# Kernel optimization log

Measured on AMD Instinct MI355X. Metric: run time of the kernel, lower is better.

## Reference

```python
import jax, jax.numpy as jnp
import numpy as np

# Hard-coded dims from the module
D, L, R, H, M, T = 64, 90, 5760, 1024, 1024, 20
N_OUT = 3
B = 64  # per-timestep batch; feature has B*T rows


def setup_inputs() -> dict:
    key = jax.random.key(0)
    ks = jax.random.split(key, 20)
    def w(i, shape, fan_in):
        return jax.random.normal(ks[i], shape, dtype=jnp.float32) * (1.0 / np.sqrt(fan_in))
    return {
        "feature": jax.random.normal(ks[0], (B * T, L, D), dtype=jnp.float32),
        # additive attention params (alpha over L locations)
        "attn_Wx": w(1, (D, D), D),
        "attn_Wh": w(2, (H, D), H),
        "attn_v": w(3, (D,), D),
        # LSTM (PyTorch gate order i,f,g,o)
        "W_ih": w(4, (4 * H, R), R),
        "W_hh": w(5, (4 * H, H), H),
        "b_ih": jnp.zeros((4 * H,), jnp.float32),
        "b_hh": jnp.zeros((4 * H,), jnp.float32),
        # output head
        "Wh_w": w(6, (M, H), H),
        "Wh_b": jnp.zeros((M,), jnp.float32),
        "Wy_w": w(7, (M, R), R),
        "Wu_w": w(8, (N_OUT, M), M),
        "Wu_b": jnp.zeros((N_OUT,), jnp.float32),
        # LSTM-state initializers
        "iWh_w": w(9, (H, D), D),
        "iWh_b": jnp.zeros((H,), jnp.float32),
        "iWc_w": w(10, (H, D), D),
        "iWc_b": jnp.zeros((H,), jnp.float32),
    }


def reference(feature, attn_Wx, attn_Wh, attn_v, W_ih, W_hh, b_ih, b_hh,
              Wh_w, Wh_b, Wy_w, Wu_w, Wu_b, iWh_w, iWh_b, iWc_w, iWc_b):
    batch = feature.shape[0] // T
    seq = feature.reshape(batch, T, L, D).transpose(1, 0, 2, 3)  # [T,B,L,D]

    # initializeLSTM (no_grad in the original -> stop_gradient)
    f0 = jnp.mean(seq[0], axis=1)                                  # [B,D]
    h0 = jax.lax.stop_gradient(jnp.tanh(f0 @ iWh_w.T + iWh_b))     # [B,H]
    c0 = jax.lax.stop_gradient(jnp.tanh(f0 @ iWc_w.T + iWc_b))     # [B,H]

    def step(carry, xt):  # xt: [B,L,D]
        h, c = carry
        # additive attention over L locations
        e = jnp.tanh(jnp.einsum('bld,da->bla', xt, attn_Wx)
                     + (h @ attn_Wh)[:, None, :]) @ attn_v          # [B,L]
        alpha = jax.nn.softmax(e, axis=1)
        visual = (xt * alpha[:, :, None]).reshape(-1, R)            # [B,R]
        # single LSTM step (PyTorch gate order i,f,g,o)
        gates = visual @ W_ih.T + b_ih + h @ W_hh.T + b_hh          # [B,4H]
        i, f, g, o = jnp.split(gates, 4, axis=-1)
        c = jax.nn.sigmoid(f) * c + jax.nn.sigmoid(i) * jnp.tanh(g)
        h = jax.nn.sigmoid(o) * jnp.tanh(c)
        # ut = Wu(Wh(h) + Wy(visual)); dropout omitted for determinism
        ut = (h @ Wh_w.T + Wh_b + visual @ Wy_w.T) @ Wu_w.T + Wu_b  # [B,n_out]
        return (h, c), ut

    _, outs = jax.lax.scan(step, (h0, c0), seq)                     # [T,B,n_out]
    return outs.transpose(1, 0, 2).reshape(batch * T, -1)
```

## Files before the change

### kernel.cpp

```cpp
#include <hip/hip_runtime.h>
#include <math.h>

typedef _Float16 half8 __attribute__((ext_vector_type(8)));
typedef _Float16 half4v __attribute__((ext_vector_type(4)));
typedef _Float16 half2v __attribute__((ext_vector_type(2)));
typedef float floatx16 __attribute__((ext_vector_type(16)));

#define TT 20
#define NB 64
#define LL 90
#define DD 64
#define RR 5760
#define HH 1024
#define NG 4096
#define KT 6784
#define CH0 90
#define CHT 106
#define SPLITK 8

__device__ __forceinline__ float sigm(float x) { return 1.f / (1.f + expf(-x)); }

__global__ __launch_bounds__(256) void k_prep(const float* __restrict__ s1, _Float16* __restrict__ d1, int n1,
                                              const float* __restrict__ s2, _Float16* __restrict__ d2, int n2,
                                              int ncb, const float* __restrict__ Wh, _Float16* __restrict__ WhT) {
    const int bid = blockIdx.x, tid = threadIdx.x;
    if (bid >= ncb) {
        const int idx = (bid - ncb) * 256 + tid;
        const int a = idx >> 8, k4 = (idx & 255) * 4;
        half4v o;
#pragma unroll
        for (int u = 0; u < 4; ++u) o[u] = (_Float16)Wh[(size_t)(k4 + u) * DD + a];
        *(half4v*)(WhT + (size_t)a * HH + k4) = o;
        return;
    }
    int i = (bid * 256 + tid) * 4;
    const float* s; _Float16* d;
    if (i < n1) { s = s1 + i; d = d1 + i; }
    else if ((i -= n1) < n2) { s = s2 + i; d = d2 + i; }
    else return;
    const float4 v = *(const float4*)s;
    half4v o;
    o[0] = (_Float16)v.x; o[1] = (_Float16)v.y;
    o[2] = (_Float16)v.z; o[3] = (_Float16)v.w;
    *(half4v*)d = o;
}

__global__ __launch_bounds__(256) void k_xproj(const float* __restrict__ feat,
                                               const float* __restrict__ Wx,
                                               _Float16* __restrict__ xp) {
    __shared__ float sWx[DD * DD];
    __shared__ float sx[16 * DD];
    const int row = blockIdx.x;
    const int tid = threadIdx.x;
    for (int e = tid * 4; e < DD * DD; e += 1024)
        *(float4*)(sWx + e) = *(const float4*)(Wx + e);
    const int a4 = tid & 15, lg = tid >> 4;
    const float* frow = feat + (size_t)row * RR;
    for (int lb = 0; lb < LL; lb += 16) {
        __syncthreads();
        { int e = tid * 4; int ls = e >> 6, dd = e & 63;
          if (lb + ls < LL) *(float4*)(sx + e) = *(const float4*)(frow + (lb + ls) * DD + dd); }
        __syncthreads();
        const int l = lb + lg;
        if (l < LL) {
            float a0 = 0, a1 = 0, a2 = 0, a3 = 0;
            for (int dd = 0; dd < DD; ++dd) {
                const float xv = sx[lg * DD + dd];
                const float4 wv = *(const float4*)(sWx + dd * DD + a4 * 4);
                a0 += xv * wv.x; a1 += xv * wv.y; a2 += xv * wv.z; a3 += xv * wv.w;
            }
            half4v o;
            o[0] = (_Float16)a0; o[1] = (_Float16)a1; o[2] = (_Float16)a2; o[3] = (_Float16)a3;
            *(half4v*)(xp + (size_t)row * RR + l * DD + a4 * 4) = o;
        }
    }
}

__global__ __launch_bounds__(256) void k_init(const float* __restrict__ feat,
        const float* __restrict__ iWh_w, const float* __restrict__ iWh_b,
        const float* __restrict__ iWc_w, const float* __restrict__ iWc_b,
        float* __restrict__ h, float* __restrict__ c, _Float16* __restrict__ h16) {
    __shared__ float f0p[4][DD];
    __shared__ float f0[DD];
    const int b = blockIdx.x, tid = threadIdx.x;
    const int dd = tid & 63, lg = tid >> 6;
    const float* frow = feat + (size_t)(b * TT) * RR;
    float p = 0;
    for (int l = lg; l < LL; l += 4) p += frow[l * DD + dd];
    f0p[lg][dd] = p;
    __syncthreads();
    if (tid < DD) f0[tid] = (f0p[0][tid] + f0p[1][tid] + f0p[2][tid] + f0p[3][tid]) * (1.0f / LL);
    __syncthreads();
    for (int o = tid; o < HH; o += 256) {
        float ah = iWh_b[o], ac = iWc_b[o];
        for (int d0 = 0; d0 < DD; d0 += 4) {
            const float4 wh = *(const float4*)(iWh_w + (size_t)o * DD + d0);
            const float4 wc = *(const float4*)(iWc_w + (size_t)o * DD + d0);
            ah += f0[d0] * wh.x + f0[d0 + 1] * wh.y + f0[d0 + 2] * wh.z + f0[d0 + 3] * wh.w;
            ac += f0[d0] * wc.x + f0[d0 + 1] * wc.y + f0[d0 + 2] * wc.z + f0[d0 + 3] * wc.w;
        }
        const float hv = tanhf(ah), cv = tanhf(ac);
        h[b * HH + o] = hv; c[b * HH + o] = cv;
        h16[b * HH + o] = (_Float16)hv;
    }
}

__global__ __launch_bounds__(512) void k_step(int t, int do_cell,
        const float* __restrict__ gpart, const float* __restrict__ b_ih,
        const float* __restrict__ b_hh, const float* __restrict__ cin,
        float* __restrict__ cout, _Float16* __restrict__ h16,
        const float* __restrict__ h0buf, const float* __restrict__ feat,
        const _Float16* __restrict__ xp, const _Float16* __restrict__ WhT,
        const float* __restrict__ v, _Float16* __restrict__ V16,
        const _Float16* __restrict__ Wyu, float* __restrict__ vpart,
        float* __restrict__ hpart) {
    __shared__ float sh[HH];
    __shared__ float hWhp[8][DD];
    __shared__ float hWh[DD];
    __shared__ float sv[DD];
    __shared__ float ep[LL][4];
    __shared__ float se[128];
    __shared__ float red[128];
    __shared__ float salpha[LL];
    __shared__ float hdr[8][6];
    const int b = blockIdx.x, tid = threadIdx.x;
    if (tid < DD) sv[tid] = v[tid];
    float hp0 = 0.f, hp1 = 0.f, hp2 = 0.f;
    float vp0 = 0.f, vp1 = 0.f, vp2 = 0.f;

    if (do_cell) {
        const int j0 = tid * 2;
        float ag[4][2];
#pragma unroll
        for (int g = 0; g < 4; ++g) { ag[g][0] = 0.f; ag[g][1] = 0.f; }
#pragma unroll
        for (int sp = 0; sp < SPLITK; ++sp) {
            const float* P = gpart + ((size_t)sp * NB + b) * NG;
#pragma unroll
            for (int g = 0; g < 4; ++g) {
                const float2 pv = *(const float2*)(P + g * HH + j0);
                ag[g][0] += pv.x; ag[g][1] += pv.y;
            }
        }
#pragma unroll
        for (int g = 0; g < 4; ++g) {
            const float2 bi = *(const float2*)(b_ih + g * HH + j0);
            const float2 bh = *(const float2*)(b_hh + g * HH + j0);
            ag[g][0] += bi.x + bh.x; ag[g][1] += bi.y + bh.y;
        }
        const float2 cold = *(const float2*)(cin + (size_t)b * HH + j0);
        float co[2] = { cold.x, cold.y };
        float2 cnew; half2v hh2;
#pragma unroll
        for (int q = 0; q < 2; ++q) {
            const float cv = sigm(ag[1][q]) * co[q] + sigm(ag[0][q]) * tanhf(ag[2][q]);
            const float hv = sigm(ag[3][q]) * tanhf(cv);
            ((float*)&cnew)[q] = cv;
            hh2[q] = (_Float16)hv;
            sh[j0 + q] = hv;
        }
        *(float2*)(cout + (size_t)b * HH + j0) = cnew;
        *(half2v*)(h16 + (size_t)b * HH + j0) = hh2;
        const float h0f = (float)hh2[0], h1f = (float)hh2[1];
        hp0 = h0f * (float)Wyu[0 * KT + RR + j0] + h1f * (float)Wyu[0 * KT + RR + j0 + 1];
        hp1 = h0f * (float)Wyu[1 * KT + RR + j0] + h1f * (float)Wyu[1 * KT + RR + j0 + 1];
        hp2 = h0f * (float)Wyu[2 * KT + RR + j0] + h1f * (float)Wyu[2 * KT + RR + j0 + 1];
    } else {
        for (int e = tid; e < HH; e += 512) sh[e] = h0buf[(size_t)b * HH + e];
    }
    __syncthreads();

    if (t < TT) {
        { const int a = tid & 63, q8 = tid >> 6;
          const _Float16* Wq = WhT + (size_t)a * HH + q8 * 128;
          const float* shq = sh + q8 * 128;
          float p = 0.f;
#pragma unroll
          for (int k = 0; k < 128; k += 8) {
              const half8 wv = *(const half8*)(Wq + k);
#pragma unroll
              for (int u = 0; u < 8; ++u) p += shq[k + u] * (float)wv[u];
          }
          hWhp[q8][a] = p; }
        __syncthreads();
        if (tid < DD) {
            float s = 0.f;
#pragma unroll
            for (int q = 0; q < 8; ++q) s += hWhp[q][tid];
            hWh[tid] = s;
        }
        __syncthreads();

        const size_t frow = (size_t)(b * TT + t) * RR;
        if (tid < 360) {
            const int l = tid >> 2, qq = tid & 3;
            const _Float16* xr = xp + frow + l * DD + qq * 16;
            const half8 x0 = *(const half8*)(xr);
            const half8 x1 = *(const half8*)(xr + 8);
            float acc = 0.f;
#pragma unroll
            for (int i = 0; i < 8; ++i)
                acc += tanhf((float)x0[i] + hWh[qq * 16 + i]) * sv[qq * 16 + i];
#pragma unroll
            for (int i = 0; i < 8; ++i)
                acc += tanhf((float)x1[i] + hWh[qq * 16 + 8 + i]) * sv[qq * 16 + 8 + i];
            ep[l][qq] = acc;
        }
        __syncthreads();
        if (tid < LL) se[tid] = ep[tid][0] + ep[tid][1] + ep[tid][2] + ep[tid][3];
        else if (tid < 128) se[tid] = -1e30f;
        __syncthreads();
        if (tid < 128) red[tid] = se[tid];
        __syncthreads();
        for (int s = 64; s; s >>= 1) { if (tid < s) red[tid] = fmaxf(red[tid], red[tid + s]); __syncthreads(); }
        const float mx = red[0];
        __syncthreads();
        float ex = 0.f;
        if (tid < LL) { ex = expf(se[tid] - mx); salpha[tid] = ex; }
        if (tid < 128) red[tid] = ex;
        __syncthreads();
        for (int s = 64; s; s >>= 1) { if (tid < s) red[tid] += red[tid + s]; __syncthreads(); }
        const float inv = 1.f / red[0];
        __syncthreads();
        if (tid < LL) salpha[tid] *= inv;
        __syncthreads();

        _Float16* vout = V16 + (size_t)b * RR;
        const float* fr = feat + frow;
        for (int e = tid * 4; e < RR; e += 2048) {
            const float4 u4 = *(const float4*)(fr + e);
            const float al = salpha[e >> 6];
            half4v o;
            o[0] = (_Float16)(u4.x * al); o[1] = (_Float16)(u4.y * al);
            o[2] = (_Float16)(u4.z * al); o[3] = (_Float16)(u4.w * al);
            *(half4v*)(vout + e) = o;
            const half4v w0 = *(const half4v*)(Wyu + e);
            const half4v w1 = *(const half4v*)(Wyu + KT + e);
            const half4v w2 = *(const half4v*)(Wyu + 2 * KT + e);
#pragma unroll
            for (int u = 0; u < 4; ++u) {
                const float xv = (float)o[u];
                vp0 += xv * (float)w0[u]; vp1 += xv * (float)w1[u]; vp2 += xv * (float)w2[u];
            }
        }
    }

    for (int o = 32; o; o >>= 1) {
        hp0 += __shfl_down(hp0, o, 64); hp1 += __shfl_down(hp1, o, 64); hp2 += __shfl_down(hp2, o, 64);
        vp0 += __shfl_down(vp0, o, 64); vp1 += __shfl_down(vp1, o, 64); vp2 += __shfl_down(vp2, o, 64);
    }
    if ((tid & 63) == 0) {
        const int w = tid >> 6;
        hdr[w][0] = hp0; hdr[w][1] = hp1; hdr[w][2] = hp2;
        hdr[w][3] = vp0; hdr[w][4] = vp1; hdr[w][5] = vp2;
    }
    __syncthreads();
    if (tid < 6) {
        float s = 0.f;
#pragma unroll
        for (int w = 0; w < 8; ++w) s += hdr[w][tid];
        if (tid < 3) { if (do_cell) hpart[((size_t)(t - 1) * NB + b) * 3 + tid] = s; }
        else         { if (t < TT)  vpart[((size_t)t * NB + b) * 3 + (tid - 3)] = s; }
    }
}

__device__ __forceinline__ void stage_tile(const char* src, size_t stride, char* lds, int ln) {
    const char* g = src + (size_t)(ln >> 3) * stride + (((ln & 7) ^ (ln >> 3)) << 4);
#pragma unroll
    for (int i = 0; i < 8; ++i)
        __builtin_amdgcn_global_load_lds(
            (const __attribute__((address_space(1))) void*)(g + (size_t)(i * 8) * stride),
            (__attribute__((address_space(3))) void*)(lds + i * 1024), 16, 0, 0);
}

struct Src2 { const char* p0; size_t s0; const char* p1; size_t s1; };

__device__ __forceinline__ const char* chunk_ptr(const Src2& s, int c, size_t& stride) {
    if (c < CH0) { stride = s.s0; return s.p0 + (size_t)c * 128; }
    stride = s.s1; return s.p1 + (size_t)(c - CH0) * 128;
}

__global__ __launch_bounds__(128) void k_gates(const _Float16* __restrict__ V16,
        const _Float16* __restrict__ h16, const _Float16* __restrict__ Wih,
        const _Float16* __restrict__ Whh, float* __restrict__ gpart) {
    __shared__ char smem[65536];
    const int bid = blockIdx.x;
    const int kb = bid >> 6;
    const int nt = ((bid & 7) << 3) | ((bid >> 3) & 7);
    const int tid = threadIdx.x, w = tid >> 6, ln = tid & 63;
    char* wlds = smem + w * 32768;

    Src2 As = { (const char*)V16, (size_t)RR * 2, (const char*)h16, (size_t)HH * 2 };
    Src2 Bs = { (const char*)(Wih + (size_t)(nt * 64) * RR), (size_t)RR * 2,
                (const char*)(Whh + (size_t)(nt * 64) * HH), (size_t)HH * 2 };

    floatx16 acc00, acc01, acc10, acc11;
#pragma unroll
    for (int i = 0; i < 16; ++i) { acc00[i] = 0.f; acc01[i] = 0.f; acc10[i] = 0.f; acc11[i] = 0.f; }

    const int start = kb * 2 + w;
    const int r = ln & 31;
    const int xsw = (r & 7) << 4;
    const int fo = (ln >> 5) * 16;
    const int rbyte = r * 128;

    int c = start, bsel = 0;
    { size_t st; const char* p = chunk_ptr(As, c, st); stage_tile(p, st, wlds, ln);
      p = chunk_ptr(Bs, c, st); stage_tile(p, st, wlds + 8192, ln); }
    while (true) {
        const int cn = c + 16;
        if (cn < CHT) {
            char* nl = wlds + ((bsel ^ 1) << 14);
            size_t st; const char* p = chunk_ptr(As, cn, st); stage_tile(p, st, nl, ln);
            p = chunk_ptr(Bs, cn, st); stage_tile(p, st, nl + 8192, ln);
            asm volatile("s_waitcnt vmcnt(16)" ::: "memory");
        } else {
            asm volatile("s_waitcnt vmcnt(0)" ::: "memory");
        }
        __builtin_amdgcn_sched_barrier(0);
        const char* LA = wlds + (bsel << 14);
        const char* LB = LA + 8192;
#pragma unroll
        for (int kk = 0; kk < 4; ++kk) {
            const int o = ((kk * 32 + fo) ^ xsw);
            const half8 a0 = *(const half8*)(LA + rbyte + o);
            const half8 a1 = *(const half8*)(LA + 4096 + rbyte + o);
            const half8 b0 = *(const half8*)(LB + rbyte + o);
            const half8 b1 = *(const half8*)(LB + 4096 + rbyte + o);
            acc00 = __builtin_amdgcn_mfma_f32_32x32x16_f16(a0, b0, acc00, 0, 0, 0);
            acc01 = __builtin_amdgcn_mfma_f32_32x32x16_f16(a0, b1, acc01, 0, 0, 0);
            acc10 = __builtin_amdgcn_mfma_f32_32x32x16_f16(a1, b0, acc10, 0, 0, 0);
            acc11 = __builtin_amdgcn_mfma_f32_32x32x16_f16(a1, b1, acc11, 0, 0, 0);
        }
        if (cn >= CHT) break;
        c = cn; bsel ^= 1;
    }
    __syncthreads();
    float* Rg = (float*)(smem + w * 16384);
    const int rbase = 4 * (ln >> 5), lr = ln & 31;
#pragma unroll
    for (int q = 0; q < 16; ++q) {
        const int row = rbase + (q & 3) + 8 * (q >> 2);
        Rg[row * 64 + lr]             = acc00[q];
        Rg[row * 64 + 32 + lr]        = acc01[q];
        Rg[(row + 32) * 64 + lr]      = acc10[q];
        Rg[(row + 32) * 64 + 32 + lr] = acc11[q];
    }
    __syncthreads();
    const float* R0 = (const float*)smem;
    const float* R1 = (const float*)(smem + 16384);
    float* Cout = gpart + (size_t)kb * (NB * NG);
    for (int e = tid * 4; e < 4096; e += 512) {
        const float4 u = *(const float4*)(R0 + e);
        const float4 v2 = *(const float4*)(R1 + e);
        float4 s2; s2.x = u.x + v2.x; s2.y = u.y + v2.y; s2.z = u.z + v2.z; s2.w = u.w + v2.w;
        const int row = e >> 6, col = e & 63;
        *(float4*)(Cout + (size_t)row * NG + nt * 64 + col) = s2;
    }
}

__global__ __launch_bounds__(256) void k_wfuse(const float* __restrict__ Wy,
        const float* __restrict__ Whw, const float* __restrict__ Wu,
        const float* __restrict__ Whb, const float* __restrict__ Wub,
        _Float16* __restrict__ Wyu16, float* __restrict__ cst) {
    __shared__ float sWu[3 * HH];
    __shared__ float part[4][3][64];
    const int tid = threadIdx.x;
    for (int e = tid * 4; e < 3 * HH; e += 1024)
        *(float4*)(sWu + e) = *(const float4*)(Wu + e);
    __syncthreads();
    if (blockIdx.x == CHT) {
        float a0 = 0, a1 = 0, a2 = 0;
        for (int m = tid; m < HH; m += 256) {
            const float wb = Whb[m];
            a0 += sWu[m] * wb; a1 += sWu[HH + m] * wb; a2 += sWu[2 * HH + m] * wb;
        }
        __shared__ float rp[3][256];
        rp[0][tid] = a0; rp[1][tid] = a1; rp[2][tid] = a2;
        __syncthreads();
        for (int s = 128; s; s >>= 1) {
            if (tid < s) { rp[0][tid] += rp[0][tid + s]; rp[1][tid] += rp[1][tid + s]; rp[2][tid] += rp[2][tid + s]; }
            __syncthreads();
        }
        if (tid < 3) cst[tid] = rp[tid][0] + Wub[tid];
        return;
    }
    const int kk = tid & 63, qm = tid >> 6;
    const int k = blockIdx.x * 64 + kk;
    const float* src; size_t ld;
    if (blockIdx.x < CH0) { src = Wy + k; ld = RR; }
    else { src = Whw + (k - RR); ld = HH; }
    float a0 = 0, a1 = 0, a2 = 0;
    for (int m = qm * 256; m < qm * 256 + 256; ++m) {
        const float val = src[(size_t)m * ld];
        a0 += sWu[m] * val; a1 += sWu[HH + m] * val; a2 += sWu[2 * HH + m] * val;
    }
    part[qm][0][kk] = a0; part[qm][1][kk] = a1; part[qm][2][kk] = a2;
    __syncthreads();
    if (tid < 192) {
        const int j = tid >> 6, k2 = tid & 63;
        const float s = part[0][j][k2] + part[1][j][k2] + part[2][j][k2] + part[3][j][k2];
        Wyu16[(size_t)j * KT + blockIdx.x * 64 + k2] = (_Float16)s;
    }
}

__global__ __launch_bounds__(256) void k_fin(const float* __restrict__ vpart,
        const float* __restrict__ hpart, const float* __restrict__ cst,
        float* __restrict__ out) {
    const int idx = blockIdx.x * 256 + threadIdx.x;
    if (idx >= TT * NB * 3) return;
    const int r = idx / 3, j = idx - r * 3;
    const int ts = r >> 6, b = r & 63;
    out[((size_t)b * TT + ts) * 3 + j] = vpart[idx] + hpart[idx] + cst[j];
}

extern "C" void kernel_launch(void* const* d_in, const int* in_sizes, int n_in,
                              void* d_out, int out_size, void* d_ws, size_t ws_size,
                              hipStream_t stream) {
    (void)in_sizes; (void)n_in; (void)out_size;
    const float* feature = (const float*)d_in[0];
    const float* attn_Wx = (const float*)d_in[1];
    const float* attn_Wh = (const float*)d_in[2];
    const float* attn_v  = (const float*)d_in[3];
    const float* W_ih    = (const float*)d_in[4];
    const float* W_hh    = (const float*)d_in[5];
    const float* b_ih    = (const float*)d_in[6];
    const float* b_hh    = (const float*)d_in[7];
    const float* Wh_w    = (const float*)d_in[8];
    const float* Wh_b    = (const float*)d_in[9];
    const float* Wy_w    = (const float*)d_in[10];
    const float* Wu_w    = (const float*)d_in[11];
    const float* Wu_b    = (const float*)d_in[12];
    const float* iWh_w   = (const float*)d_in[13];
    const float* iWh_b   = (const float*)d_in[14];
    const float* iWc_w   = (const float*)d_in[15];
    const float* iWc_b   = (const float*)d_in[16];
    float* out = (float*)d_out;

    char* ws = (char*)d_ws;
    size_t off = 0;
    auto alloc = [&](size_t bytes) { void* p = ws + off; off += (bytes + 255) & ~(size_t)255; return p; };
    _Float16* Wih16 = (_Float16*)alloc((size_t)NG * RR * 2);
    _Float16* Whh16 = (_Float16*)alloc((size_t)NG * HH * 2);
    _Float16* WhT16 = (_Float16*)alloc((size_t)DD * HH * 2);
    _Float16* xp16  = (_Float16*)alloc((size_t)1280 * RR * 2);
    _Float16* V16   = (_Float16*)alloc((size_t)NB * RR * 2);
    float*    hbuf  = (float*)alloc((size_t)NB * HH * 4);
    float*    cb0   = (float*)alloc((size_t)NB * HH * 4);
    float*    cb1   = (float*)alloc((size_t)NB * HH * 4);
    _Float16* h16   = (_Float16*)alloc((size_t)NB * HH * 2);
    float*    gpart = (float*)alloc((size_t)SPLITK * NB * NG * 4);
    _Float16* Wyu16 = (_Float16*)alloc((size_t)3 * KT * 2);
    float*    vpart = (float*)alloc((size_t)TT * NB * 3 * 4);
    float*    hpart = (float*)alloc((size_t)TT * NB * 3 * 4);
    float*    cstb  = (float*)alloc(16);
    if (ws_size < off) return;

    const int nconv = NG * RR + NG * HH;
    const int ncb = (nconv / 4 + 255) / 256;
    k_prep<<<ncb + 64, 256, 0, stream>>>(W_ih, Wih16, NG * RR, W_hh, Whh16, NG * HH,
                                         ncb, attn_Wh, WhT16);
    k_xproj<<<1280, 256, 0, stream>>>(feature, attn_Wx, xp16);
    k_wfuse<<<CHT + 1, 256, 0, stream>>>(Wy_w, Wh_w, Wu_w, Wh_b, Wu_b, Wyu16, cstb);
    k_init<<<64, 256, 0, stream>>>(feature, iWh_w, iWh_b, iWc_w, iWc_b, hbuf, cb0, h16);

    k_step<<<64, 512, 0, stream>>>(0, 0, gpart, b_ih, b_hh, cb0, cb1, h16, hbuf,
                                   feature, xp16, WhT16, attn_v, V16, Wyu16,
                                   vpart, hpart);
    for (int t = 0; t < TT; ++t) {
        k_gates<<<512, 128, 0, stream>>>(V16, h16, Wih16, Whh16, gpart);
        const float* cin = (t & 1) ? cb1 : cb0;
        float* cou       = (t & 1) ? cb0 : cb1;
        k_step<<<64, 512, 0, stream>>>(t + 1, 1, gpart, b_ih, b_hh, cin, cou, h16, hbuf,
                                       feature, xp16, WhT16, attn_v, V16, Wyu16,
                                       vpart, hpart);
    }

    k_fin<<<15, 256, 0, stream>>>(vpart, hpart, cstb, out);
}
```

Measured before the change: 687.3 us.

## Overlap per-step Wx projection with gate GEMM and merge prep kernels

The full 1280-row Wx projection is no longer precomputed up front. Each gates launch now gets 64 extra blocks that compute the next timestep's projection into a double-buffered 64-row slice, overlapping it with the GEMM. The gate GEMM is restructured into 128 blocks of 4 waves that share a staged A tile and write split-K partials directly, and the small prep kernels and the final output kernel are folded into one prep launch and into the last step. This cuts launch count and prep work, but puts extra projection work on the per-step critical path and lowers GEMM block parallelism from 512 to 128 blocks.

```diff
diff --git a/kernel.cpp b/kernel.cpp
--- a/kernel.cpp
+++ b/kernel.cpp
@@ -20,20 +20,9 @@
 
 __device__ __forceinline__ float sigm(float x) { return 1.f / (1.f + expf(-x)); }
 
-__global__ __launch_bounds__(256) void k_prep(const float* __restrict__ s1, _Float16* __restrict__ d1, int n1,
-                                              const float* __restrict__ s2, _Float16* __restrict__ d2, int n2,
-                                              int ncb, const float* __restrict__ Wh, _Float16* __restrict__ WhT) {
-    const int bid = blockIdx.x, tid = threadIdx.x;
-    if (bid >= ncb) {
-        const int idx = (bid - ncb) * 256 + tid;
-        const int a = idx >> 8, k4 = (idx & 255) * 4;
-        half4v o;
-#pragma unroll
-        for (int u = 0; u < 4; ++u) o[u] = (_Float16)Wh[(size_t)(k4 + u) * DD + a];
-        *(half4v*)(WhT + (size_t)a * HH + k4) = o;
-        return;
-    }
-    int i = (bid * 256 + tid) * 4;
+__global__ __launch_bounds__(256) void k_conv2(const float* __restrict__ s1, _Float16* __restrict__ d1, int n1,
+                                               const float* __restrict__ s2, _Float16* __restrict__ d2, int n2) {
+    int i = (blockIdx.x * 256 + threadIdx.x) * 4;
     const float* s; _Float16* d;
     if (i < n1) { s = s1 + i; d = d1 + i; }
     else if ((i -= n1) < n2) { s = s2 + i; d = d2 + i; }
@@ -45,63 +34,254 @@
     *(half4v*)d = o;
 }
 
-__global__ __launch_bounds__(256) void k_xproj(const float* __restrict__ feat,
-                                               const float* __restrict__ Wx,
-                                               _Float16* __restrict__ xp) {
-    __shared__ float sWx[DD * DD];
-    __shared__ float sx[16 * DD];
-    const int row = blockIdx.x;
-    const int tid = threadIdx.x;
-    for (int e = tid * 4; e < DD * DD; e += 1024)
-        *(float4*)(sWx + e) = *(const float4*)(Wx + e);
-    const int a4 = tid & 15, lg = tid >> 4;
-    const float* frow = feat + (size_t)row * RR;
-    for (int lb = 0; lb < LL; lb += 16) {
-        __syncthreads();
-        { int e = tid * 4; int ls = e >> 6, dd = e & 63;
-          if (lb + ls < LL) *(float4*)(sx + e) = *(const float4*)(frow + (lb + ls) * DD + dd); }
-        __syncthreads();
-        const int l = lb + lg;
-        if (l < LL) {
-            float a0 = 0, a1 = 0, a2 = 0, a3 = 0;
-            for (int dd = 0; dd < DD; ++dd) {
-                const float xv = sx[lg * DD + dd];
-                const float4 wv = *(const float4*)(sWx + dd * DD + a4 * 4);
-                a0 += xv * wv.x; a1 += xv * wv.y; a2 += xv * wv.z; a3 += xv * wv.w;
-            }
-            half4v o;
-            o[0] = (_Float16)a0; o[1] = (_Float16)a1; o[2] = (_Float16)a2; o[3] = (_Float16)a3;
-            *(half4v*)(xp + (size_t)row * RR + l * DD + a4 * 4) = o;
-        }
-    }
-}
-
-__global__ __launch_bounds__(256) void k_init(const float* __restrict__ feat,
-        const float* __restrict__ iWh_w, const float* __restrict__ iWh_b,
-        const float* __restrict__ iWc_w, const float* __restrict__ iWc_b,
-        float* __restrict__ h, float* __restrict__ c, _Float16* __restrict__ h16) {
-    __shared__ float f0p[4][DD];
-    __shared__ float f0[DD];
-    const int b = blockIdx.x, tid = threadIdx.x;
-    const int dd = tid & 63, lg = tid >> 6;
-    const float* frow = feat + (size_t)(b * TT) * RR;
-    float p = 0;
-    for (int l = lg; l < LL; l += 4) p += frow[l * DD + dd];
-    f0p[lg][dd] = p;
-    __syncthreads();
-    if (tid < DD) f0[tid] = (f0p[0][tid] + f0p[1][tid] + f0p[2][tid] + f0p[3][tid]) * (1.0f / LL);
-    __syncthreads();
-    for (int o = tid; o < HH; o += 256) {
-        float ah = iWh_b[o], ac = iWc_b[o];
-        for (int d0 = 0; d0 < DD; d0 += 4) {
-            const float4 wh = *(const float4*)(iWh_w + (size_t)o * DD + d0);
-            const float4 wc = *(const float4*)(iWc_w + (size_t)o * DD + d0);
-            ah += f0[d0] * wh.x + f0[d0 + 1] * wh.y + f0[d0 + 2] * wh.z + f0[d0 + 3] * wh.w;
-            ac += f0[d0] * wc.x + f0[d0 + 1] * wc.y + f0[d0 + 2] * wc.z + f0[d0 + 3] * wc.w;
-        }
-        const float hv = tanhf(ah), cv = tanhf(ac);
-        h[b * HH + o] = hv; c[b * HH + o] = cv;
-        h16[b * HH + o] = (_Float16)hv;
+__global__ __launch_bounds__(256) void k_small_prep(
+        const float* __restrict__ Wh, _Float16* __restrict__ WhT,
+        const float* __restrict__ Wy, const float* __restrict__ Whw,
+        const float* __restrict__ Wu, const float* __restrict__ Whb,
+        const float* __restrict__ Wub, _Float16* __restrict__ Wyu16,
+        float* __restrict__ cst,
+        const float* __restrict__ feat, const float* __restrict__ iWh_w,
+        const float* __restrict__ iWh_b, const float* __restrict__ iWc_w,
+        const float* __restrict__ iWc_b, float* __restrict__ hbuf,
+        float* __restrict__ c0buf, _Float16* __restrict__ h16,
+        const float* __restrict__ Wx, _Float16* __restrict__ xpA) {
+    __shared__ char pm[20480];
+    const int bid = blockIdx.x, tid = threadIdx.x;
+
+    if (bid < 64) {
+        const int idx = bid * 256 + tid;
+        const int a = idx >> 8, k4 = (idx & 255) * 4;
+        half4v o;
+#pragma unroll
+        for (int u = 0; u < 4; ++u) o[u] = (_Float16)Wh[(size_t)(k4 + u) * DD + a];
+        *(half4v*)(WhT + (size_t)a * HH + k4) = o;
+        return;
+    }
+    if (bid < 171) {
+        const int wb = bid - 64;
+        float* sWu = (float*)pm;
+        float* part = sWu + 3 * HH;
+        float* rp = part + 768;
+        for (int e = tid * 4; e < 3 * HH; e += 1024)
+            *(float4*)(sWu + e) = *(const float4*)(Wu + e);
+        __syncthreads();
+        if (wb == CHT) {
+            float a0 = 0, a1 = 0, a2 = 0;
+            for (int m = tid; m < HH; m += 256) {
+                const float w = Whb[m];
+                a0 += sWu[m] * w; a1 += sWu[HH + m] * w; a2 += sWu[2 * HH + m] * w;
+            }
+            rp[tid] = a0; rp[256 + tid] = a1; rp[512 + tid] = a2;
+            __syncthreads();
+            for (int s = 128; s; s >>= 1) {
+                if (tid < s) { rp[tid] += rp[tid + s]; rp[256 + tid] += rp[256 + tid + s]; rp[512 + tid] += rp[512 + tid + s]; }
+                __syncthreads();
+            }
+            if (tid < 3) cst[tid] = rp[tid * 256] + Wub[tid];
+            return;
+        }
+        const int kk = tid & 63, qm = tid >> 6;
+        const int k = wb * 64 + kk;
+        const float* src; size_t ld;
+        if (wb < CH0) { src = Wy + k; ld = RR; }
+        else { src = Whw + (k - RR); ld = HH; }
+        float a0 = 0, a1 = 0, a2 = 0;
+        for (int m = qm * 256; m < qm * 256 + 256; ++m) {
+            const float val = src[(size_t)m * ld];
+            a0 += sWu[m] * val; a1 += sWu[HH + m] * val; a2 += sWu[2 * HH + m] * val;
+        }
+        part[(qm * 3 + 0) * 64 + kk] = a0;
+        part[(qm * 3 + 1) * 64 + kk] = a1;
+        part[(qm * 3 + 2) * 64 + kk] = a2;
+        __syncthreads();
+        if (tid < 192) {
+            const int j = tid >> 6, k2 = tid & 63;
+            float s = 0.f;
+#pragma unroll
+            for (int qm2 = 0; qm2 < 4; ++qm2) s += part[(qm2 * 3 + j) * 64 + k2];
+            Wyu16[(size_t)j * KT + wb * 64 + k2] = (_Float16)s;
+        }
+        return;
+    }
+    if (bid < 235) {
+        const int b = bid - 171;
+        float* f0p = (float*)pm;
+        float* f0 = f0p + 256;
+        const int dd = tid & 63, lg = tid >> 6;
+        const float* frow = feat + (size_t)(b * TT) * RR;
+        float p = 0;
+        for (int l = lg; l < LL; l += 4) p += frow[l * DD + dd];
+        f0p[lg * 64 + dd] = p;
+        __syncthreads();
+        if (tid < DD) f0[tid] = (f0p[tid] + f0p[64 + tid] + f0p[128 + tid] + f0p[192 + tid]) * (1.0f / LL);
+        __syncthreads();
+        for (int o = tid; o < HH; o += 256) {
+            float ah = iWh_b[o], ac = iWc_b[o];
+            for (int d0 = 0; d0 < DD; d0 += 4) {
+                const float4 wh = *(const float4*)(iWh_w + (size_t)o * DD + d0);
+                const float4 wc = *(const float4*)(iWc_w + (size_t)o * DD + d0);
+                ah += f0[d0] * wh.x + f0[d0 + 1] * wh.y + f0[d0 + 2] * wh.z + f0[d0 + 3] * wh.w;
+                ac += f0[d0] * wc.x + f0[d0 + 1] * wc.y + f0[d0 + 2] * wc.z + f0[d0 + 3] * wc.w;
+            }
+            const float hv = tanhf(ah), cv = tanhf(ac);
+            hbuf[b * HH + o] = hv; c0buf[b * HH + o] = cv;
+            h16[b * HH + o] = (_Float16)hv;
+        }
+        return;
+    }
+    {
+        const int b = bid - 235;
+        float* sWx = (float*)pm;
+        float* sx = sWx + 4096;
+        for (int e = tid * 4; e < DD * DD; e += 1024)
+            *(float4*)(sWx + e) = *(const float4*)(Wx + e);
+        const int a4 = tid & 15, lg = tid >> 4;
+        const float* frow = feat + (size_t)(b * TT) * RR;
+        _Float16* xr = xpA + (size_t)b * RR;
+        for (int lb = 0; lb < LL; lb += 16) {
+            __syncthreads();
+            { int e = tid * 4; int ls = e >> 6, dd = e & 63;
+              if (lb + ls < LL) *(float4*)(sx + e) = *(const float4*)(frow + (lb + ls) * DD + dd); }
+            __syncthreads();
+            const int l = lb + lg;
+            if (l < LL) {
+                float a0 = 0, a1 = 0, a2 = 0, a3 = 0;
+                for (int dd = 0; dd < DD; ++dd) {
+                    const float xv = sx[lg * DD + dd];
+                    const float4 wv = *(const float4*)(sWx + dd * DD + a4 * 4);
+                    a0 += xv * wv.x; a1 += xv * wv.y; a2 += xv * wv.z; a3 += xv * wv.w;
+                }
+                half4v o;
+                o[0] = (_Float16)a0; o[1] = (_Float16)a1; o[2] = (_Float16)a2; o[3] = (_Float16)a3;
+                *(half4v*)(xr + l * DD + a4 * 4) = o;
+            }
+        }
+    }
+}
+
+__device__ __forceinline__ void stage_tile(const char* src, size_t stride, char* lds, int ln) {
+    const char* g = src + (size_t)(ln >> 3) * stride + (((ln & 7) ^ (ln >> 3)) << 4);
+#pragma unroll
+    for (int i = 0; i < 8; ++i)
+        __builtin_amdgcn_global_load_lds(
+            (const __attribute__((address_space(1))) void*)(g + (size_t)(i * 8) * stride),
+            (__attribute__((address_space(3))) void*)(lds + i * 1024), 16, 0, 0);
+}
+
+struct Src2 { const char* p0; size_t s0; const char* p1; size_t s1; };
+
+__device__ __forceinline__ const char* chunk_ptr(const Src2& s, int c, size_t& stride) {
+    if (c < CH0) { stride = s.s0; return s.p0 + (size_t)c * 128; }
+    stride = s.s1; return s.p1 + (size_t)(c - CH0) * 128;
+}
+
+__global__ __launch_bounds__(256) void k_gates(int t,
+        const _Float16* __restrict__ V16, const _Float16* __restrict__ h16,
+        const _Float16* __restrict__ Wih, const _Float16* __restrict__ Whh,
+        float* __restrict__ gpart, const float* __restrict__ feat,
+        const float* __restrict__ Wx, _Float16* __restrict__ xpw) {
+    __shared__ char smem[81920];
+    const int bid = blockIdx.x, tid = threadIdx.x;
+
+    if (bid >= 128) {
+        if (t + 1 >= TT) return;
+        float* sWx = (float*)smem;
+        float* sx = sWx + 4096;
+        const int b = bid - 128;
+        for (int e = tid * 4; e < DD * DD; e += 1024)
+            *(float4*)(sWx + e) = *(const float4*)(Wx + e);
+        const int a4 = tid & 15, lg = tid >> 4;
+        const float* frow = feat + ((size_t)b * TT + t + 1) * RR;
+        _Float16* xr = xpw + (size_t)b * RR;
+        for (int lb = 0; lb < LL; lb += 16) {
+            __syncthreads();
+            { int e = tid * 4; int ls = e >> 6, dd = e & 63;
+              if (lb + ls < LL) *(float4*)(sx + e) = *(const float4*)(frow + (lb + ls) * DD + dd); }
+            __syncthreads();
+            const int l = lb + lg;
+            if (l < LL) {
+                float a0 = 0, a1 = 0, a2 = 0, a3 = 0;
+                for (int dd = 0; dd < DD; ++dd) {
+                    const float xv = sx[lg * DD + dd];
+                    const float4 wv = *(const float4*)(sWx + dd * DD + a4 * 4);
+                    a0 += xv * wv.x; a1 += xv * wv.y; a2 += xv * wv.z; a3 += xv * wv.w;
+                }
+                half4v o;
+                o[0] = (_Float16)a0; o[1] = (_Float16)a1; o[2] = (_Float16)a2; o[3] = (_Float16)a3;
+                *(half4v*)(xr + l * DD + a4 * 4) = o;
+            }
+        }
+        return;
+    }
+
+    const int kb = bid & 7;
+    const int nt = bid >> 3;
+    const int w = tid >> 6, ln = tid & 63;
+    const int n0w = nt * 256 + w * 64;
+
+    Src2 As = { (const char*)V16, (size_t)RR * 2, (const char*)h16, (size_t)HH * 2 };
+    Src2 Bs = { (const char*)(Wih + (size_t)n0w * RR), (size_t)RR * 2,
+                (const char*)(Whh + (size_t)n0w * HH), (size_t)HH * 2 };
+
+    floatx16 acc00, acc01, acc10, acc11;
+#pragma unroll
+    for (int i = 0; i < 16; ++i) { acc00[i] = 0.f; acc01[i] = 0.f; acc10[i] = 0.f; acc11[i] = 0.f; }
+
+    const int r = ln & 31;
+    const int xsw = (r & 7) << 4;
+    const int fo = (ln >> 5) * 16;
+    const int rbyte = r * 128;
+
+    int c = kb, cur = 0;
+    {
+        char* bb = smem;
+        size_t st; const char* p;
+        if (w == 0) { p = chunk_ptr(As, c, st); stage_tile(p, st, bb, ln); }
+        p = chunk_ptr(Bs, c, st); stage_tile(p, st, bb + 8192 + w * 8192, ln);
+    }
+    while (true) {
+        const int cn = c + SPLITK;
+        if (cn < CHT) {
+            char* nb = smem + ((cur ^ 1) * 40960);
+            size_t st; const char* p;
+            if (w == 0) { p = chunk_ptr(As, cn, st); stage_tile(p, st, nb, ln); }
+            p = chunk_ptr(Bs, cn, st); stage_tile(p, st, nb + 8192 + w * 8192, ln);
+            if (w == 0) asm volatile("s_waitcnt vmcnt(16)" ::: "memory");
+            else        asm volatile("s_waitcnt vmcnt(8)" ::: "memory");
+        } else {
+            asm volatile("s_waitcnt vmcnt(0)" ::: "memory");
+        }
+        __builtin_amdgcn_sched_barrier(0);
+        __builtin_amdgcn_s_barrier();
+        __builtin_amdgcn_sched_barrier(0);
+        const char* LA = smem + cur * 40960;
+        const char* LB = LA + 8192 + w * 8192;
+#pragma unroll
+        for (int kk = 0; kk < 4; ++kk) {
+            const int o = ((kk * 32 + fo) ^ xsw);
+            const half8 a0 = *(const half8*)(LA + rbyte + o);
+            const half8 a1 = *(const half8*)(LA + 4096 + rbyte + o);
+            const half8 b0 = *(const half8*)(LB + rbyte + o);
+            const half8 b1 = *(const half8*)(LB + 4096 + rbyte + o);
+            acc00 = __builtin_amdgcn_mfma_f32_32x32x16_f16(a0, b0, acc00, 0, 0, 0);
+            acc01 = __builtin_amdgcn_mfma_f32_32x32x16_f16(a0, b1, acc01, 0, 0, 0);
+            acc10 = __builtin_amdgcn_mfma_f32_32x32x16_f16(a1, b0, acc10, 0, 0, 0);
+            acc11 = __builtin_amdgcn_mfma_f32_32x32x16_f16(a1, b1, acc11, 0, 0, 0);
+        }
+        if (cn >= CHT) break;
+        __builtin_amdgcn_sched_barrier(0);
+        __builtin_amdgcn_s_barrier();
+        c = cn; cur ^= 1;
+    }
+    float* P = gpart + (size_t)kb * (NB * NG);
+    const int rbase = 4 * (ln >> 5);
+#pragma unroll
+    for (int q = 0; q < 16; ++q) {
+        const int row = rbase + (q & 3) + 8 * (q >> 2);
+        P[(size_t)row * NG + n0w + r]             = acc00[q];
+        P[(size_t)row * NG + n0w + 32 + r]        = acc01[q];
+        P[(size_t)(row + 32) * NG + n0w + r]      = acc10[q];
+        P[(size_t)(row + 32) * NG + n0w + 32 + r] = acc11[q];
     }
 }
 
@@ -113,7 +293,8 @@
         const _Float16* __restrict__ xp, const _Float16* __restrict__ WhT,
         const float* __restrict__ v, _Float16* __restrict__ V16,
         const _Float16* __restrict__ Wyu, float* __restrict__ vpart,
-        float* __restrict__ hpart) {
+        float* __restrict__ hpart, const float* __restrict__ cst,
+        float* __restrict__ out) {
     __shared__ float sh[HH];
     __shared__ float hWhp[8][DD];
     __shared__ float hWh[DD];
@@ -123,6 +304,7 @@
     __shared__ float red[128];
     __shared__ float salpha[LL];
     __shared__ float hdr[8][6];
+    __shared__ float hloc[3];
     const int b = blockIdx.x, tid = threadIdx.x;
     if (tid < DD) sv[tid] = v[tid];
     float hp0 = 0.f, hp1 = 0.f, hp2 = 0.f;
@@ -191,10 +373,9 @@
         }
         __syncthreads();
 
-        const size_t frow = (size_t)(b * TT + t) * RR;
         if (tid < 360) {
             const int l = tid >> 2, qq = tid & 3;
-            const _Float16* xr = xp + frow + l * DD + qq * 16;
+            const _Float16* xr = xp + (size_t)b * RR + l * DD + qq * 16;
             const half8 x0 = *(const half8*)(xr);
             const half8 x1 = *(const half8*)(xr + 8);
             float acc = 0.f;
@@ -226,7 +407,7 @@
         __syncthreads();
 
         _Float16* vout = V16 + (size_t)b * RR;
-        const float* fr = feat + frow;
+        const float* fr = feat + ((size_t)b * TT + t) * RR;
         for (int e = tid * 4; e < RR; e += 2048) {
             const float4 u4 = *(const float4*)(fr + e);
             const float al = salpha[e >> 6];
@@ -250,168 +431,29 @@
         vp0 += __shfl_down(vp0, o, 64); vp1 += __shfl_down(vp1, o, 64); vp2 += __shfl_down(vp2, o, 64);
     }
     if ((tid & 63) == 0) {
-        const int w = tid >> 6;
-        hdr[w][0] = hp0; hdr[w][1] = hp1; hdr[w][2] = hp2;
-        hdr[w][3] = vp0; hdr[w][4] = vp1; hdr[w][5] = vp2;
+        const int wv = tid >> 6;
+        hdr[wv][0] = hp0; hdr[wv][1] = hp1; hdr[wv][2] = hp2;
+        hdr[wv][3] = vp0; hdr[wv][4] = vp1; hdr[wv][5] = vp2;
     }
     __syncthreads();
     if (tid < 6) {
         float s = 0.f;
 #pragma unroll
-        for (int w = 0; w < 8; ++w) s += hdr[w][tid];
-        if (tid < 3) { if (do_cell) hpart[((size_t)(t - 1) * NB + b) * 3 + tid] = s; }
-        else         { if (t < TT)  vpart[((size_t)t * NB + b) * 3 + (tid - 3)] = s; }
-    }
-}
-
-__device__ __forceinline__ void stage_tile(const char* src, size_t stride, char* lds, int ln) {
-    const char* g = src + (size_t)(ln >> 3) * stride + (((ln & 7) ^ (ln >> 3)) << 4);
-#pragma unroll
-    for (int i = 0; i < 8; ++i)
-        __builtin_amdgcn_global_load_lds(
-            (const __attribute__((address_space(1))) void*)(g + (size_t)(i * 8) * stride),
-            (__attribute__((address_space(3))) void*)(lds + i * 1024), 16, 0, 0);
-}
-
-struct Src2 { const char* p0; size_t s0; const char* p1; size_t s1; };
-
-__device__ __forceinline__ const char* chunk_ptr(const Src2& s, int c, size_t& stride) {
-    if (c < CH0) { stride = s.s0; return s.p0 + (size_t)c * 128; }
-    stride = s.s1; return s.p1 + (size_t)(c - CH0) * 128;
-}
-
-__global__ __launch_bounds__(128) void k_gates(const _Float16* __restrict__ V16,
-        const _Float16* __restrict__ h16, const _Float16* __restrict__ Wih,
-        const _Float16* __restrict__ Whh, float* __restrict__ gpart) {
-    __shared__ char smem[65536];
-    const int bid = blockIdx.x;
-    const int kb = bid >> 6;
-    const int nt = ((bid & 7) << 3) | ((bid >> 3) & 7);
-    const int tid = threadIdx.x, w = tid >> 6, ln = tid & 63;
-    char* wlds = smem + w * 32768;
-
-    Src2 As = { (const char*)V16, (size_t)RR * 2, (const char*)h16, (size_t)HH * 2 };
-    Src2 Bs = { (const char*)(Wih + (size_t)(nt * 64) * RR), (size_t)RR * 2,
-                (const char*)(Whh + (size_t)(nt * 64) * HH), (size_t)HH * 2 };
-
-    floatx16 acc00, acc01, acc10, acc11;
-#pragma unroll
-    for (int i = 0; i < 16; ++i) { acc00[i] = 0.f; acc01[i] = 0.f; acc10[i] = 0.f; acc11[i] = 0.f; }
-
-    const int start = kb * 2 + w;
-    const int r = ln & 31;
-    const int xsw = (r & 7) << 4;
-    const int fo = (ln >> 5) * 16;
-    const int rbyte = r * 128;
-
-    int c = start, bsel = 0;
-    { size_t st; const char* p = chunk_ptr(As, c, st); stage_tile(p, st, wlds, ln);
-      p = chunk_ptr(Bs, c, st); stage_tile(p, st, wlds + 8192, ln); }
-    while (true) {
-        const int cn = c + 16;
-        if (cn < CHT) {
-            char* nl = wlds + ((bsel ^ 1) << 14);
-            size_t st; const char* p = chunk_ptr(As, cn, st); stage_tile(p, st, nl, ln);
-            p = chunk_ptr(Bs, cn, st); stage_tile(p, st, nl + 8192, ln);
-            asm volatile("s_waitcnt vmcnt(16)" ::: "memory");
+        for (int wv = 0; wv < 8; ++wv) s += hdr[wv][tid];
+        if (tid < 3) {
+            if (do_cell) { hpart[((size_t)(t - 1) * NB + b) * 3 + tid] = s; hloc[tid] = s; }
         } else {
-            asm volatile("s_waitcnt vmcnt(0)" ::: "memory");
-        }
-        __builtin_amdgcn_sched_barrier(0);
-        const char* LA = wlds + (bsel << 14);
-        const char* LB = LA + 8192;
-#pragma unroll
-        for (int kk = 0; kk < 4; ++kk) {
-            const int o = ((kk * 32 + fo) ^ xsw);
-            const half8 a0 = *(const half8*)(LA + rbyte + o);
-            const half8 a1 = *(const half8*)(LA + 4096 + rbyte + o);
-            const half8 b0 = *(const half8*)(LB + rbyte + o);
-            const half8 b1 = *(const half8*)(LB + 4096 + rbyte + o);
-            acc00 = __builtin_amdgcn_mfma_f32_32x32x16_f16(a0, b0, acc00, 0, 0, 0);
-            acc01 = __builtin_amdgcn_mfma_f32_32x32x16_f16(a0, b1, acc01, 0, 0, 0);
-            acc10 = __builtin_amdgcn_mfma_f32_32x32x16_f16(a1, b0, acc10, 0, 0, 0);
-            acc11 = __builtin_amdgcn_mfma_f32_32x32x16_f16(a1, b1, acc11, 0, 0, 0);
-        }
-        if (cn >= CHT) break;
-        c = cn; bsel ^= 1;
+            if (t < TT) vpart[((size_t)t * NB + b) * 3 + (tid - 3)] = s;
+        }
     }
     __syncthreads();
-    float* Rg = (float*)(smem + w * 16384);
-    const int rbase = 4 * (ln >> 5), lr = ln & 31;
-#pragma unroll
-    for (int q = 0; q < 16; ++q) {
-        const int row = rbase + (q & 3) + 8 * (q >> 2);
-        Rg[row * 64 + lr]             = acc00[q];
-        Rg[row * 64 + 32 + lr]        = acc01[q];
-        Rg[(row + 32) * 64 + lr]      = acc10[q];
-        Rg[(row + 32) * 64 + 32 + lr] = acc11[q];
-    }
-    __syncthreads();
-    const float* R0 = (const float*)smem;
-    const float* R1 = (const float*)(smem + 16384);
-    float* Cout = gpart + (size_t)kb * (NB * NG);
-    for (int e = tid * 4; e < 4096; e += 512) {
-        const float4 u = *(const float4*)(R0 + e);
-        const float4 v2 = *(const float4*)(R1 + e);
-        float4 s2; s2.x = u.x + v2.x; s2.y = u.y + v2.y; s2.z = u.z + v2.z; s2.w = u.w + v2.w;
-        const int row = e >> 6, col = e & 63;
-        *(float4*)(Cout + (size_t)row * NG + nt * 64 + col) = s2;
-    }
-}
-
-__global__ __launch_bounds__(256) void k_wfuse(const float* __restrict__ Wy,
-        const float* __restrict__ Whw, const float* __restrict__ Wu,
-        const float* __restrict__ Whb, const float* __restrict__ Wub,
-        _Float16* __restrict__ Wyu16, float* __restrict__ cst) {
-    __shared__ float sWu[3 * HH];
-    __shared__ float part[4][3][64];
-    const int tid = threadIdx.x;
-    for (int e = tid * 4; e < 3 * HH; e += 1024)
-        *(float4*)(sWu + e) = *(const float4*)(Wu + e);
-    __syncthreads();
-    if (blockIdx.x == CHT) {
-        float a0 = 0, a1 = 0, a2 = 0;
-        for (int m = tid; m < HH; m += 256) {
-            const float wb = Whb[m];
-            a0 += sWu[m] * wb; a1 += sWu[HH + m] * wb; a2 += sWu[2 * HH + m] * wb;
-        }
-        __shared__ float rp[3][256];
-        rp[0][tid] = a0; rp[1][tid] = a1; rp[2][tid] = a2;
-        __syncthreads();
-        for (int s = 128; s; s >>= 1) {
-            if (tid < s) { rp[0][tid] += rp[0][tid + s]; rp[1][tid] += rp[1][tid + s]; rp[2][tid] += rp[2][tid + s]; }
-            __syncthreads();
-        }
-        if (tid < 3) cst[tid] = rp[tid][0] + Wub[tid];
-        return;
-    }
-    const int kk = tid & 63, qm = tid >> 6;
-    const int k = blockIdx.x * 64 + kk;
-    const float* src; size_t ld;
-    if (blockIdx.x < CH0) { src = Wy + k; ld = RR; }
-    else { src = Whw + (k - RR); ld = HH; }
-    float a0 = 0, a1 = 0, a2 = 0;
-    for (int m = qm * 256; m < qm * 256 + 256; ++m) {
-        const float val = src[(size_t)m * ld];
-        a0 += sWu[m] * val; a1 += sWu[HH + m] * val; a2 += sWu[2 * HH + m] * val;
-    }
-    part[qm][0][kk] = a0; part[qm][1][kk] = a1; part[qm][2][kk] = a2;
-    __syncthreads();
-    if (tid < 192) {
-        const int j = tid >> 6, k2 = tid & 63;
-        const float s = part[0][j][k2] + part[1][j][k2] + part[2][j][k2] + part[3][j][k2];
-        Wyu16[(size_t)j * KT + blockIdx.x * 64 + k2] = (_Float16)s;
-    }
-}
-
-__global__ __launch_bounds__(256) void k_fin(const float* __restrict__ vpart,
-        const float* __restrict__ hpart, const float* __restrict__ cst,
-        float* __restrict__ out) {
-    const int idx = blockIdx.x * 256 + threadIdx.x;
-    if (idx >= TT * NB * 3) return;
-    const int r = idx / 3, j = idx - r * 3;
-    const int ts = r >> 6, b = r & 63;
-    out[((size_t)b * TT + ts) * 3 + j] = vpart[idx] + hpart[idx] + cst[j];
+    if (t == TT) {
+        for (int i = tid; i < TT * 3; i += 512) {
+            const int ts = i / 3, j = i - ts * 3;
+            const float hp = (ts == TT - 1) ? hloc[j] : hpart[((size_t)ts * NB + b) * 3 + j];
+            out[((size_t)b * TT + ts) * 3 + j] = vpart[((size_t)ts * NB + b) * 3 + j] + hp + cst[j];
+        }
+    }
 }
 
 extern "C" void kernel_launch(void* const* d_in, const int* in_sizes, int n_in,
@@ -443,7 +485,8 @@
     _Float16* Wih16 = (_Float16*)alloc((size_t)NG * RR * 2);
     _Float16* Whh16 = (_Float16*)alloc((size_t)NG * HH * 2);
     _Float16* WhT16 = (_Float16*)alloc((size_t)DD * HH * 2);
-    _Float16* xp16  = (_Float16*)alloc((size_t)1280 * RR * 2);
+    _Float16* xpA   = (_Float16*)alloc((size_t)NB * RR * 2);
+    _Float16* xpB   = (_Float16*)alloc((size_t)NB * RR * 2);
     _Float16* V16   = (_Float16*)alloc((size_t)NB * RR * 2);
     float*    hbuf  = (float*)alloc((size_t)NB * HH * 4);
     float*    cb0   = (float*)alloc((size_t)NB * HH * 4);
@@ -457,24 +500,23 @@
     if (ws_size < off) return;
 
     const int nconv = NG * RR + NG * HH;
-    const int ncb = (nconv / 4 + 255) / 256;
-    k_prep<<<ncb + 64, 256, 0, stream>>>(W_ih, Wih16, NG * RR, W_hh, Whh16, NG * HH,
-                                         ncb, attn_Wh, WhT16);
-    k_xproj<<<1280, 256, 0, stream>>>(feature, attn_Wx, xp16);
-    k_wfuse<<<CHT + 1, 256, 0, stream>>>(Wy_w, Wh_w, Wu_w, Wh_b, Wu_b, Wyu16, cstb);
-    k_init<<<64, 256, 0, stream>>>(feature, iWh_w, iWh_b, iWc_w, iWc_b, hbuf, cb0, h16);
+    k_conv2<<<(nconv / 4 + 255) / 256, 256, 0, stream>>>(W_ih, Wih16, NG * RR,
+                                                         W_hh, Whh16, NG * HH);
+    k_small_prep<<<299, 256, 0, stream>>>(attn_Wh, WhT16, Wy_w, Wh_w, Wu_w, Wh_b, Wu_b,
+                                          Wyu16, cstb, feature, iWh_w, iWh_b, iWc_w,
+                                          iWc_b, hbuf, cb0, h16, attn_Wx, xpA);
 
     k_step<<<64, 512, 0, stream>>>(0, 0, gpart, b_ih, b_hh, cb0, cb1, h16, hbuf,
-                                   feature, xp16, WhT16, attn_v, V16, Wyu16,
-                                   vpart, hpart);
+                                   feature, xpA, WhT16, attn_v, V16, Wyu16,
+                                   vpart, hpart, cstb, out);
     for (int t = 0; t < TT; ++t) {
-        k_gates<<<512, 128, 0, stream>>>(V16, h16, Wih16, Whh16, gpart);
+        _Float16* xpw = ((t + 1) & 1) ? xpB : xpA;
+        k_gates<<<192, 256, 0, stream>>>(t, V16, h16, Wih16, Whh16, gpart,
+                                         feature, attn_Wx, xpw);
         const float* cin = (t & 1) ? cb1 : cb0;
         float* cou       = (t & 1) ? cb0 : cb1;
         k_step<<<64, 512, 0, stream>>>(t + 1, 1, gpart, b_ih, b_hh, cin, cou, h16, hbuf,
-                                       feature, xp16, WhT16, attn_v, V16, Wyu16,
-                                       vpart, hpart);
-    }
-
-    k_fin<<<15, 256, 0, stream>>>(vpart, hpart, cstb, out);
-}
+                                       feature, xpw, WhT16, attn_v, V16, Wyu16,
+                                       vpart, hpart, cstb, out);
+    }
+}
```

New measurement: 743.8 us. 1.08x slower.
